# Performance work log

Measured on AMD Instinct MI355X. Metric: run time of the kernel, lower is better.

## Reference

```python
import jax, jax.numpy as jnp
import numpy as np

# Conv2dfft forward (no spectral compression: preserve_energy=None, index_back=None, out_size=None)
# Implements cross-correlation (DL convolution) via rfft2 / irfft2, matching the torch module's
# padding and output-size logic:
#   out_H = H - HH + 1 + 2*pad ; init_fft = H + 2*pad + max(out_H, HH) - 1

PAD = 1  # padding from init_kwargs


def setup_inputs() -> dict:
    key = jax.random.key(0)
    k1, k2, k3 = jax.random.split(key, 3)
    x = jax.random.normal(k1, (32, 128, 32, 32), dtype=jnp.float32)
    w = jax.random.normal(k2, (128, 128, 3, 3), dtype=jnp.float32) * 0.1
    b = jax.random.normal(k3, (128,), dtype=jnp.float32)
    return {"x": x, "w": w, "b": b}


def reference(x, w, b):
    N, C, H, W = x.shape
    F, _, HH, WW = w.shape
    out_H = H - HH + 1 + 2 * PAD
    out_W = W - WW + 1 + 2 * PAD
    init_fft_H = H + 2 * PAD + max(out_H, HH) - 1  # 65
    init_fft_W = W + 2 * PAD + max(out_W, WW) - 1  # 65

    # pad input: explicit conv padding + zero-pad up to FFT grid
    fft_pad_H = init_fft_H - 2 * PAD - H
    fft_pad_W = init_fft_W - 2 * PAD - W
    px = jnp.pad(x, ((0, 0), (0, 0), (PAD, PAD + fft_pad_H), (PAD, PAD + fft_pad_W)))
    pw = jnp.pad(w, ((0, 0), (0, 0), (0, init_fft_H - HH), (0, init_fft_W - WW)))

    xfft = jnp.fft.rfft2(px)                     # [N,C,65,33] complex64
    yfft = jnp.fft.rfft2(pw)                     # [F,C,65,33] complex64

    # cross-correlation: multiply by conj(filter fft), accumulate over input channels
    prod = jnp.einsum('nchw,fchw->nfhw', xfft, jnp.conj(yfft))
    full = jnp.fft.irfft2(prod, s=(init_fft_H, init_fft_W))  # [N,F,65,65]
    out = full[:, :, :out_H, :out_W] + b[None, :, None, None]
    return out
```

## Files before the change

kernel.cpp:

```cpp
#include <hip/hip_runtime.h>


typedef __attribute__((ext_vector_type(8))) short bf16x8;
typedef __attribute__((ext_vector_type(4))) float f32x4;

#define N_IMG 32
#define C_IN  128
#define F_OUT 128
#define HW    32
#define HPAD  34

__device__ __forceinline__ unsigned short f2bf(float f) {
    union { float f; unsigned u; } v; v.f = f;
    unsigned r = v.u + 0x7fffu + ((v.u >> 16) & 1u);
    return (unsigned short)(r >> 16);
}

__global__ __launch_bounds__(256) void pack_x_kernel(const float* __restrict__ x,
                                                     unsigned short* __restrict__ xp) {
    __shared__ unsigned short tile[C_IN * HPAD];
    const int n   = blockIdx.x / HPAD;
    const int hp  = blockIdx.x - n * HPAD;
    const int tid = threadIdx.x;
    const unsigned base_out = (unsigned)(n * HPAD + hp) * (HPAD * C_IN);
    if (hp >= 1 && hp <= 32) {
        const int h = hp - 1;
        #pragma unroll
        for (int i = 0; i < 16; ++i) {
            int idx = tid + i * 256;
            int c = idx >> 5, w = idx & 31;
            tile[c * HPAD + (w + 1)] = f2bf(x[((n * C_IN + c) * HW + h) * HW + w]);
        }
        if (tid < C_IN) { tile[tid * HPAD] = 0; tile[tid * HPAD + 33] = 0; }
        __syncthreads();
        #pragma unroll
        for (int i = 0; i < 17; ++i) {
            int idx = tid + i * 256;
            int wp = idx >> 7, c = idx & 127;
            xp[base_out + (unsigned)idx] = tile[c * HPAD + wp];
        }
    } else {
        #pragma unroll
        for (int i = 0; i < 17; ++i) {
            int idx = tid + i * 256;
            xp[base_out + (unsigned)idx] = 0;
        }
    }
}

__global__ __launch_bounds__(256) void pack_w_kernel(const float* __restrict__ w,
                                                     unsigned short* __restrict__ wpk) {
    int idx = blockIdx.x * 256 + threadIdx.x;
    int ci = idx & 31;
    int f  = (idx >> 5) & 127;
    int u  = idx >> 12;
    int cc = u / 9;
    int t  = u - cc * 9;
    wpk[idx] = f2bf(w[(f * C_IN + cc * 32 + ci) * 9 + t]);
}

__global__ __launch_bounds__(256, 2) void conv_gemm_kernel(
    const unsigned short* __restrict__ xp,
    const unsigned short* __restrict__ wpk,
    const float* __restrict__ bias,
    float* __restrict__ out)
{
    __shared__ alignas(16) unsigned short lds_x[208 * C_IN];

    const int tid  = threadIdx.x;
    const int lane = tid & 63;
    const int wave = tid >> 6;
    const int qk   = lane >> 4;
    const int l15  = lane & 15;

    const int fh   = blockIdx.x & 1;
    const int band = (blockIdx.x >> 1) & 7;
    const int n    = blockIdx.x >> 4;
    const int f0   = fh * 64;
    const int h0   = band * 4;

    const unsigned short* xbase = xp + (unsigned)((n * HPAD + h0) * HPAD) * C_IN;
    #pragma unroll
    for (int i = 0; i < 13; ++i) {
        int p = tid + i * 256;
        int row = p >> 4;  if (row > 203) row = 203;
        int lc = (p ^ row) & 15;
        const unsigned short* src = xbase + row * C_IN + lc * 8;
        __builtin_amdgcn_global_load_lds(
            (const __attribute__((address_space(1))) void*)src,
            (__attribute__((address_space(3))) void*)(&lds_x[p * 8]),
            16, 0, 0);
    }

    f32x4 acc[4][2];
    #pragma unroll
    for (int mi = 0; mi < 4; ++mi)
        #pragma unroll
        for (int ni = 0; ni < 2; ++ni)
            acc[mi][ni] = (f32x4){0.f, 0.f, 0.f, 0.f};

    const unsigned short* wbase = wpk + f0 * 32 + l15 * 32 + qk * 8;

    const int rrb0 = wave * HPAD + l15;
    const int rrb1 = wave * HPAD + 16 + l15;

    __syncthreads();

    #pragma unroll
    for (int cc = 0; cc < 4; ++cc) {
        #pragma unroll
        for (int tap = 0; tap < 9; ++tap) {
            const int r = tap / 3, s = tap - 3 * (tap / 3);
            bf16x8 af[4], bf[2];
            #pragma unroll
            for (int mi = 0; mi < 4; ++mi)
                af[mi] = *(const bf16x8*)(wbase + cc * 36864 + tap * 4096 + mi * 512);
            {
                int rr0 = rrb0 + r * HPAD + s;
                int ph0 = (cc * 4 + qk) ^ (rr0 & 15);
                bf[0] = *(const bf16x8*)&lds_x[rr0 * C_IN + ph0 * 8];
                int rr1 = rrb1 + r * HPAD + s;
                int ph1 = (cc * 4 + qk) ^ (rr1 & 15);
                bf[1] = *(const bf16x8*)&lds_x[rr1 * C_IN + ph1 * 8];
            }
            #pragma unroll
            for (int mi = 0; mi < 4; ++mi)
                #pragma unroll
                for (int ni = 0; ni < 2; ++ni)
                    acc[mi][ni] = __builtin_amdgcn_mfma_f32_16x16x32_bf16(
                        af[mi], bf[ni], acc[mi][ni], 0, 0, 0);
        }
    }

    const int h = h0 + wave;
    #pragma unroll
    for (int mi = 0; mi < 4; ++mi) {
        const int f_base = f0 + mi * 16 + qk * 4;
        float bv[4];
        #pragma unroll
        for (int r2 = 0; r2 < 4; ++r2) bv[r2] = bias[f_base + r2];
        #pragma unroll
        for (int ni = 0; ni < 2; ++ni) {
            const int w2 = ni * 16 + l15;
            #pragma unroll
            for (int r2 = 0; r2 < 4; ++r2) {
                out[((unsigned)(n * F_OUT + f_base + r2) * HW + h) * HW + w2] =
                    acc[mi][ni][r2] + bv[r2];
            }
        }
    }
}

extern "C" void kernel_launch(void* const* d_in, const int* in_sizes, int n_in,
                              void* d_out, int out_size, void* d_ws, size_t ws_size,
                              hipStream_t stream) {
    const float* x = (const float*)d_in[0];
    const float* w = (const float*)d_in[1];
    const float* b = (const float*)d_in[2];
    float* out = (float*)d_out;

    unsigned short* xp  = (unsigned short*)d_ws;
    unsigned short* wpk = xp + (size_t)N_IMG * HPAD * HPAD * C_IN;

    pack_x_kernel<<<N_IMG * HPAD, 256, 0, stream>>>(x, xp);
    pack_w_kernel<<<576, 256, 0, stream>>>(w, wpk);
    conv_gemm_kernel<<<512, 256, 0, stream>>>(xp, wpk, b, out);
}
```

Measured before the change: 101.0 us.

## Stage weights in double-buffered LDS and cover both filter halves per block

Each block now computes all 128 filters for its 4-row band, with the waves split into filter half × row pair, so the input tile in LDS is loaded once per band instead of twice. Weights are repacked into an MFMA-friendly layout and streamed into two LDS buffers with async global_load_lds, overlapping the next tap group's load with compute, instead of every wave loading them straight from global memory. Each wave holds 4×4 accumulators, doubling register use, and the grid halves to 256 blocks at 1 block per SM, which lowers occupancy and parallelism.

```diff
diff --git a/kernel.cpp b/kernel.cpp
--- a/kernel.cpp
+++ b/kernel.cpp
@@ -51,21 +51,23 @@
 __global__ __launch_bounds__(256) void pack_w_kernel(const float* __restrict__ w,
                                                      unsigned short* __restrict__ wpk) {
     int idx = blockIdx.x * 256 + threadIdx.x;
-    int ci = idx & 31;
-    int f  = (idx >> 5) & 127;
-    int u  = idx >> 12;
-    int cc = u / 9;
-    int t  = u - cc * 9;
-    wpk[idx] = f2bf(w[(f * C_IN + cc * 32 + ci) * 9 + t]);
+    int c8  = idx & 7;
+    int f   = (idx >> 3) & 127;
+    int qk  = (idx >> 10) & 3;
+    int u   = idx >> 12;
+    int cc  = u / 9;
+    int tap = u - cc * 9;
+    wpk[idx] = f2bf(w[(f * C_IN + cc * 32 + qk * 8 + c8) * 9 + tap]);
 }
 
-__global__ __launch_bounds__(256, 2) void conv_gemm_kernel(
+__global__ __launch_bounds__(256, 1) void conv_gemm_kernel(
     const unsigned short* __restrict__ xp,
     const unsigned short* __restrict__ wpk,
     const float* __restrict__ bias,
     float* __restrict__ out)
 {
     __shared__ alignas(16) unsigned short lds_x[208 * C_IN];
+    __shared__ alignas(16) unsigned short lds_w[2][5 * 4096];
 
     const int tid  = threadIdx.x;
     const int lane = tid & 63;
@@ -73,13 +75,13 @@
     const int qk   = lane >> 4;
     const int l15  = lane & 15;
 
-    const int fh   = blockIdx.x & 1;
-    const int band = (blockIdx.x >> 1) & 7;
-    const int n    = blockIdx.x >> 4;
+    const int band = blockIdx.x & 7;
+    const int n    = blockIdx.x >> 3;
+    const int fh   = wave >> 1;
+    const int rp   = wave & 1;
     const int f0   = fh * 64;
-    const int h0   = band * 4;
 
-    const unsigned short* xbase = xp + (unsigned)((n * HPAD + h0) * HPAD) * C_IN;
+    const unsigned short* xbase = xp + (unsigned)((n * HPAD + band * 4) * HPAD) * C_IN;
     #pragma unroll
     for (int i = 0; i < 13; ++i) {
         int p = tid + i * 256;
@@ -92,47 +94,69 @@
             16, 0, 0);
     }
 
-    f32x4 acc[4][2];
+    #define STAGE_W(ccv, t0v, ntv, bufv) do {                                   \
+        const unsigned short* wsrc = wpk + ((ccv) * 9 + (t0v)) * 4096;          \
+        _Pragma("unroll")                                                       \
+        for (int j_ = 0; j_ < 2 * (ntv); ++j_) {                                \
+            int p_ = tid + j_ * 256;                                            \
+            __builtin_amdgcn_global_load_lds(                                   \
+                (const __attribute__((address_space(1))) void*)(wsrc + p_ * 8), \
+                (__attribute__((address_space(3))) void*)(&lds_w[bufv][p_ * 8]),\
+                16, 0, 0);                                                      \
+        }                                                                       \
+    } while (0)
+
+    STAGE_W(0, 0, 5, 0);
+
+    f32x4 acc[4][4];
     #pragma unroll
     for (int mi = 0; mi < 4; ++mi)
         #pragma unroll
-        for (int ni = 0; ni < 2; ++ni)
+        for (int ni = 0; ni < 4; ++ni)
             acc[mi][ni] = (f32x4){0.f, 0.f, 0.f, 0.f};
 
-    const unsigned short* wbase = wpk + f0 * 32 + l15 * 32 + qk * 8;
+    int rrb[4];
+    #pragma unroll
+    for (int ni = 0; ni < 4; ++ni)
+        rrb[ni] = (rp * 2 + (ni >> 1)) * HPAD + (ni & 1) * 16 + l15;
 
-    const int rrb0 = wave * HPAD + l15;
-    const int rrb1 = wave * HPAD + 16 + l15;
+    const int af_base = qk * 1024 + (f0 + l15) * 8;
 
     __syncthreads();
 
-    #pragma unroll
+    #define COMPUTE(bufv, T0, NT, ccv)                                          \
+        _Pragma("unroll")                                                       \
+        for (int tl = 0; tl < (NT); ++tl) {                                     \
+            const int tap = (T0) + tl;                                          \
+            const int r = tap / 3, s = tap - 3 * (tap / 3);                     \
+            bf16x8 af[4], bf[4];                                                \
+            _Pragma("unroll")                                                   \
+            for (int mi = 0; mi < 4; ++mi)                                      \
+                af[mi] = *(const bf16x8*)&lds_w[bufv][tl * 4096 + af_base + mi * 128]; \
+            _Pragma("unroll")                                                   \
+            for (int ni = 0; ni < 4; ++ni) {                                    \
+                int rr = rrb[ni] + r * HPAD + s;                                \
+                int ph = ((ccv) * 4 + qk) ^ (rr & 15);                          \
+                bf[ni] = *(const bf16x8*)&lds_x[rr * C_IN + ph * 8];            \
+            }                                                                   \
+            _Pragma("unroll")                                                   \
+            for (int mi = 0; mi < 4; ++mi)                                      \
+                _Pragma("unroll")                                               \
+                for (int ni = 0; ni < 4; ++ni)                                  \
+                    acc[mi][ni] = __builtin_amdgcn_mfma_f32_16x16x32_bf16(      \
+                        af[mi], bf[ni], acc[mi][ni], 0, 0, 0);                  \
+        }
+
     for (int cc = 0; cc < 4; ++cc) {
-        #pragma unroll
-        for (int tap = 0; tap < 9; ++tap) {
-            const int r = tap / 3, s = tap - 3 * (tap / 3);
-            bf16x8 af[4], bf[2];
-            #pragma unroll
-            for (int mi = 0; mi < 4; ++mi)
-                af[mi] = *(const bf16x8*)(wbase + cc * 36864 + tap * 4096 + mi * 512);
-            {
-                int rr0 = rrb0 + r * HPAD + s;
-                int ph0 = (cc * 4 + qk) ^ (rr0 & 15);
-                bf[0] = *(const bf16x8*)&lds_x[rr0 * C_IN + ph0 * 8];
-                int rr1 = rrb1 + r * HPAD + s;
-                int ph1 = (cc * 4 + qk) ^ (rr1 & 15);
-                bf[1] = *(const bf16x8*)&lds_x[rr1 * C_IN + ph1 * 8];
-            }
-            #pragma unroll
-            for (int mi = 0; mi < 4; ++mi)
-                #pragma unroll
-                for (int ni = 0; ni < 2; ++ni)
-                    acc[mi][ni] = __builtin_amdgcn_mfma_f32_16x16x32_bf16(
-                        af[mi], bf[ni], acc[mi][ni], 0, 0, 0);
-        }
+        STAGE_W(cc, 5, 4, 1);
+        COMPUTE(0, 0, 5, cc);
+        __syncthreads();
+        if (cc < 3) STAGE_W(cc + 1, 0, 5, 0);
+        COMPUTE(1, 5, 4, cc);
+        __syncthreads();
     }
 
-    const int h = h0 + wave;
+    const int h0 = band * 4 + rp * 2;
     #pragma unroll
     for (int mi = 0; mi < 4; ++mi) {
         const int f_base = f0 + mi * 16 + qk * 4;
@@ -140,8 +164,9 @@
         #pragma unroll
         for (int r2 = 0; r2 < 4; ++r2) bv[r2] = bias[f_base + r2];
         #pragma unroll
-        for (int ni = 0; ni < 2; ++ni) {
-            const int w2 = ni * 16 + l15;
+        for (int ni = 0; ni < 4; ++ni) {
+            const int h  = h0 + (ni >> 1);
+            const int w2 = (ni & 1) * 16 + l15;
             #pragma unroll
             for (int r2 = 0; r2 < 4; ++r2) {
                 out[((unsigned)(n * F_OUT + f_base + r2) * HW + h) * HW + w2] =
@@ -149,6 +174,8 @@
             }
         }
     }
+    #undef STAGE_W
+    #undef COMPUTE
 }
 
 extern "C" void kernel_launch(void* const* d_in, const int* in_sizes, int n_in,
@@ -164,5 +191,5 @@
 
     pack_x_kernel<<<N_IMG * HPAD, 256, 0, stream>>>(x, xp);
     pack_w_kernel<<<576, 256, 0, stream>>>(w, wpk);
-    conv_gemm_kernel<<<512, 256, 0, stream>>>(xp, wpk, b, out);
+    conv_gemm_kernel<<<N_IMG * 8, 256, 0, stream>>>(xp, wpk, b, out);
 }
```

Measured after the change: 91.50 us. -9.4%, faster.
